# Optimization experiments

Measured on AMD Instinct MI355X. Metric: run time of the kernel, lower is better.

## Reference

```python
import jax, jax.numpy as jnp
import numpy as np

EPS = 1e-6

def _det3(m):
    return (m[..., 0, 0] * m[..., 1, 1] * m[..., 2, 2]
            + m[..., 0, 1] * m[..., 1, 2] * m[..., 2, 0]
            + m[..., 1, 0] * m[..., 2, 1] * m[..., 0, 2]
            - m[..., 2, 0] * m[..., 1, 1] * m[..., 0, 2]
            - m[..., 0, 0] * m[..., 2, 1] * m[..., 1, 2]
            - m[..., 1, 0] * m[..., 0, 1] * m[..., 2, 2])

def _inv3(m):
    a, b, c = m[..., 0, 0], m[..., 0, 1], m[..., 0, 2]
    d, e, f = m[..., 1, 0], m[..., 1, 1], m[..., 1, 2]
    g, h, i = m[..., 2, 0], m[..., 2, 1], m[..., 2, 2]
    adj = jnp.stack([
        jnp.stack([e * i - f * h, c * h - b * i, b * f - c * e], -1),
        jnp.stack([f * g - d * i, a * i - c * g, c * d - a * f], -1),
        jnp.stack([d * h - e * g, b * g - a * h, a * e - b * d], -1)], -2)
    return adj / _det3(m)[..., None, None]

def setup_inputs() -> dict:
    key = jax.random.key(0)
    ks = jax.random.split(key, 12)
    N, B, DH = 100000, 2048, 256
    idx = jnp.sort(jnp.concatenate([jnp.arange(B, dtype=jnp.int32),
                                    jax.random.randint(ks[0], (N - B,), 0, B, dtype=jnp.int32)]))
    return {
        "t": jax.random.uniform(ks[1], (B, 1), jnp.float32, 0.01, 0.99),
        "h": jax.random.normal(ks[2], (N, DH), jnp.float32),
        "pos": jax.random.normal(ks[3], (N, 3), jnp.float32),
        "eps_h": jax.random.normal(ks[4], (N, DH), jnp.float32),
        "eps_pos": jax.random.normal(ks[5], (N, 3), jnp.float32),
        "gparam_h": jax.random.normal(ks[6], (1, 1), jnp.float32),
        "gparam_pos": jax.random.normal(ks[7], (1, 1), jnp.float32),
        "W_mu": jax.random.normal(ks[8], (DH, DH), jnp.float32) / np.sqrt(DH),
        "W_r1": jax.random.normal(ks[9], (DH, 2 * DH), jnp.float32) / np.sqrt(DH),
        "W_r2": jax.random.normal(ks[10], (2 * DH, DH), jnp.float32) / np.sqrt(2 * DH),
        "index": idx,
        "num_graphs": B,
    }


def _forward(t, h, pos, eps_h, eps_pos, gparam_h, gparam_pos, W_mu, W_r1, W_r2, index, B):
    eye = jnp.eye(3, dtype=h.dtype)
    seg_sum = lambda x: jax.ops.segment_sum(x, index, num_segments=B)
    counts = seg_sum(jnp.ones((index.shape[0],), h.dtype))  # [B]

    def scatter_center(x):  # x - per-graph mean, gathered back
        mean = seg_sum(x) / counts[:, None]
        return x - mean[index]

    # volatility g(t): per-graph, gathered to nodes
    g_h = (0.1 + jax.nn.softplus(gparam_h) * t)[index]      # [N,1]
    g_pos = (0.1 + jax.nn.softplus(gparam_pos) * t)[index]  # [N,1]

    def f_net(t_, hh, pp):  # surrogate forward transformation f
        tn = t_[index]                                      # [N,1]
        mu_h = (hh @ W_mu) * (1.0 - tn)
        sigma_h = 0.1 + 0.9 * tn                            # [N,1]
        mu_pos = pp * (1.0 - tn)
        nrm = pp / (jnp.linalg.norm(pp, axis=-1, keepdims=True) + EPS)
        a = (0.2 + 0.8 * tn)[..., None]                     # [N,1,1]
        b = (0.1 * tn)[..., None]
        U = a * eye + b * (nrm[:, :, None] * nrm[:, None, :])  # [N,3,3]
        return mu_h, sigma_h, mu_pos, U

    def z_pos_fn(mu, U, eps):
        return mu + scatter_center(jnp.einsum('nij,nj->ni', U, eps))

    def score_pos_fn(eps, U, inv_U=None, C=None):
        if inv_U is None or C is None:
            inv_U = _inv3(U)
            inv_V = _inv3(seg_sum(inv_U))
            C = inv_V[index] @ (inv_U - eye)
        y = jnp.einsum('nji,nj->ni', inv_U, eps)
        ybar = seg_sum(y)
        c = jnp.einsum('nji,nj->ni', C, ybar[index])
        return scatter_center(c - y)  # zero_cog_score=True

    def solve_pos_fn(U, prel):
        inv_U = _inv3(U)
        inv_V = _inv3(seg_sum(inv_U))
        C = inv_V[index] @ (inv_U - eye)
        c = seg_sum(jnp.einsum('nij,nj->ni', C, prel))[index]
        eps = jnp.einsum('nij,nj->ni', inv_U, prel - c)
        return eps, inv_U, C

    bdrift = lambda dz, score, g: dz - 0.5 * g ** 2 * score

    # ---- target backward drift (time_derivative via jvp over t) ----
    (mu_h, sig_h, mu_p, U), (dmu_h, dsig_h, dmu_p, dU) = jax.jvp(
        lambda tt: f_net(tt, h, pos), (t,), (jnp.ones_like(t),))
    z_h = mu_h + sig_h * eps_h
    dz_h = dmu_h + dsig_h * eps_h
    z_p = z_pos_fn(mu_p, U, eps_pos)
    dz_p = z_pos_fn(dmu_p, dU, eps_pos)
    tgt_h = bdrift(dz_h, -eps_h / sig_h, g_h)
    tgt_p = bdrift(dz_p, score_pos_fn(eps_pos, U), g_pos)

    # ---- approximate backward drift ('x0' parameterization) ----
    h_r = jnp.tanh(z_h @ W_r1) @ W_r2   # reconstructor r
    pos_r = z_p * 0.9
    (mu_h2, sig_h2, mu_p2, U2), (dmu_h2, dsig_h2, dmu_p2, dU2) = jax.jvp(
        lambda tt: f_net(tt, h_r, pos_r), (t,), (jnp.ones_like(t),))
    eps_h2 = (z_h - mu_h2) / sig_h2
    eps_p2, inv_U2, C2 = solve_pos_fn(U2, z_p - mu_p2)
    dz_h2 = dmu_h2 + dsig_h2 * eps_h2
    dz_p2 = z_pos_fn(dmu_p2, dU2, eps_p2)
    apx_h = bdrift(dz_h2, -eps_h2 / sig_h2, g_h)
    apx_p = bdrift(dz_p2, score_pos_fn(eps_p2, U2, inv_U2, C2), g_pos)

    # ---- 'simple' loss: mse(approx/g, target/g) ----
    loss_h = jnp.mean(((apx_h - tgt_h) / g_h) ** 2)
    loss_p = jnp.mean(((apx_p - tgt_p) / g_pos) ** 2)
    return loss_h, loss_p


def reference(t, h, pos, eps_h, eps_pos, gparam_h, gparam_pos, W_mu, W_r1, W_r2, index, num_graphs):
    return _forward(t, h, pos, eps_h, eps_pos, gparam_h, gparam_pos, W_mu, W_r1, W_r2, index, num_graphs)
```

## Files before the change

### kernel.cpp

```cpp
#include <hip/hip_runtime.h>
#include <math.h>

#define NTHREADS 256
#define EPSC 1e-6f
#define NPL 3

typedef short bf16x8 __attribute__((ext_vector_type(8)));
typedef float f32x4  __attribute__((ext_vector_type(4)));

__device__ __forceinline__ ushort f2bf(float x) {
  union { float f; unsigned u; } v; v.f = x;
  unsigned r = v.u + 0x7FFFu + ((v.u >> 16) & 1u);
  return (ushort)(r >> 16);
}
__device__ __forceinline__ float bf2f(ushort x) {
  union { unsigned u; float f; } v; v.u = ((unsigned)x) << 16;
  return v.f;
}
__device__ __forceinline__ float tanh_fast(float x) {
  float xc = fminf(fmaxf(x, -15.f), 15.f);
  float e = __expf(2.f * xc);
  return (e - 1.f) / (e + 1.f);
}

__device__ __forceinline__ void inv3x3(const float m[9], float o[9]) {
  float a=m[0],b=m[1],c=m[2],d=m[3],e=m[4],f=m[5],g=m[6],h=m[7],i=m[8];
  float det = a*e*i + b*f*g + d*h*c - g*e*c - a*h*f - d*b*i;
  float r = 1.0f/det;
  o[0]=(e*i-f*h)*r; o[1]=(c*h-b*i)*r; o[2]=(b*f-c*e)*r;
  o[3]=(f*g-d*i)*r; o[4]=(a*i-c*g)*r; o[5]=(c*d-a*f)*r;
  o[6]=(d*h-e*g)*r; o[7]=(b*g-a*h)*r; o[8]=(a*e-b*d)*r;
}

__device__ __forceinline__ float wred(float v) {
#pragma unroll
  for (int o = 32; o > 0; o >>= 1) v += __shfl_xor(v, o, 64);
  return v;
}

__device__ __forceinline__ void block_reduce_atomic(double v, double* target) {
#pragma unroll
  for (int off = 32; off > 0; off >>= 1) v += __shfl_down(v, off, 64);
  __shared__ double sm[NTHREADS/64];
  int lane = threadIdx.x & 63, wv = threadIdx.x >> 6;
  if (lane == 0) sm[wv] = v;
  __syncthreads();
  if (threadIdx.x == 0) {
    double s = 0.0;
#pragma unroll
    for (int i = 0; i < NTHREADS/64; ++i) s += sm[i];
    atomicAdd(target, s);
  }
}

__global__ __launch_bounds__(64) void pos_fused(
    int N, const float* __restrict__ pos, const float* __restrict__ epsp,
    const int* __restrict__ index, const float* __restrict__ t,
    const float* __restrict__ gpp, double* __restrict__ lossp)
{
  const int b = blockIdx.x;
  const int lane = threadIdx.x;

  int lo = 0, hi = N;
  while (lo < hi) { int mid = (lo + hi) >> 1; if (index[mid] < b) lo = mid + 1; else hi = mid; }
  const int start = lo;
  hi = N;
  while (lo < hi) { int mid = (lo + hi) >> 1; if (index[mid] < b + 1) lo = mid + 1; else hi = mid; }
  const int end = lo;
  const int cnt = end - start;
  const float fn = (float)cnt, rc = 1.0f / fn;

  const float tn  = t[b];
  const float a1  = 0.2f + 0.8f*tn, b1 = 0.1f*tn;
  const float omt = 1.0f - tn;
  const float sp  = log1pf(expf(gpp[0]));
  const float gp  = 0.1f + sp*tn;
  const float hg  = 0.5f*gp*gp;
  const float rgp = 1.0f/gp;
  const float pscale = 1.0f - 0.9f*omt;

  float iU[NPL][9], yv[NPL][3], wv[NPL][3], dwv[NPL][3], pv[NPL][3];
  float Vs[9] = {0}, wb[3] = {0}, dwb[3] = {0}, yb[3] = {0};
#pragma unroll
  for (int k = 0; k < NPL; ++k) {
    const int n = start + k*64 + lane;
    if (n < end) {
      const float px = pos[3*(size_t)n+0], py = pos[3*(size_t)n+1], pz = pos[3*(size_t)n+2];
      const float ex = epsp[3*(size_t)n+0], ey = epsp[3*(size_t)n+1], ez = epsp[3*(size_t)n+2];
      pv[k][0]=px; pv[k][1]=py; pv[k][2]=pz;
      const float pn = sqrtf(px*px+py*py+pz*pz) + EPSC;
      const float nx = px/pn, ny = py/pn, nz = pz/pn;
      const float nd = nx*ex + ny*ey + nz*ez;
      wv[k][0]=a1*ex + b1*nd*nx; wv[k][1]=a1*ey + b1*nd*ny; wv[k][2]=a1*ez + b1*nd*nz;
      dwv[k][0]=0.8f*ex + 0.1f*nd*nx; dwv[k][1]=0.8f*ey + 0.1f*nd*ny; dwv[k][2]=0.8f*ez + 0.1f*nd*nz;
      const float U[9] = { a1 + b1*nx*nx, b1*nx*ny,      b1*nx*nz,
                           b1*ny*nx,      a1 + b1*ny*ny, b1*ny*nz,
                           b1*nz*nx,      b1*nz*ny,      a1 + b1*nz*nz };
      inv3x3(U, iU[k]);
      yv[k][0] = iU[k][0]*ex + iU[k][3]*ey + iU[k][6]*ez;
      yv[k][1] = iU[k][1]*ex + iU[k][4]*ey + iU[k][7]*ez;
      yv[k][2] = iU[k][2]*ex + iU[k][5]*ey + iU[k][8]*ez;
#pragma unroll
      for (int j = 0; j < 9; ++j) Vs[j] += iU[k][j];
#pragma unroll
      for (int j = 0; j < 3; ++j) { wb[j]+=wv[k][j]; dwb[j]+=dwv[k][j]; yb[j]+=yv[k][j]; }
    }
  }
#pragma unroll
  for (int j = 0; j < 9; ++j) Vs[j] = wred(Vs[j]);
#pragma unroll
  for (int j = 0; j < 3; ++j) { wb[j]=wred(wb[j]); dwb[j]=wred(dwb[j]); yb[j]=wred(yb[j]); }

  float iV[9]; inv3x3(Vs, iV);
  float wm[3], dwm[3], u1[3], s1m[3];
#pragma unroll
  for (int i = 0; i < 3; ++i) { wm[i] = wb[i]*rc; dwm[i] = dwb[i]*rc; }
#pragma unroll
  for (int i = 0; i < 3; ++i) u1[i] = iV[0*3+i]*yb[0] + iV[1*3+i]*yb[1] + iV[2*3+i]*yb[2];
#pragma unroll
  for (int i = 0; i < 3; ++i) {
    const float csy = Vs[0*3+i]*u1[0] + Vs[1*3+i]*u1[1] + Vs[2*3+i]*u1[2] - fn*u1[i];
    s1m[i] = (csy - yb[i]) * rc;
  }

  float tg[NPL][3], zp[NPL][3], iU2[NPL][9], qv[NPL][3];
  float Vs2[9] = {0}, qs[3] = {0}, ps[3] = {0};
#pragma unroll
  for (int k = 0; k < NPL; ++k) {
    const int n = start + k*64 + lane;
    if (n < end) {
#pragma unroll
      for (int i = 0; i < 3; ++i) {
        const float c1 = iU[k][0*3+i]*u1[0] + iU[k][1*3+i]*u1[1] + iU[k][2*3+i]*u1[2] - u1[i];
        const float score1 = c1 - yv[k][i] - s1m[i];
        tg[k][i] = -pv[k][i] + dwv[k][i] - dwm[i] - hg*score1;
        zp[k][i] = pv[k][i]*omt + wv[k][i] - wm[i];
      }
      const float rx = 0.9f*zp[k][0], ry = 0.9f*zp[k][1], rz = 0.9f*zp[k][2];
      const float rn = sqrtf(rx*rx+ry*ry+rz*rz) + EPSC;
      const float nx = rx/rn, ny = ry/rn, nz = rz/rn;
      const float U2[9] = { a1 + b1*nx*nx, b1*nx*ny,      b1*nx*nz,
                            b1*ny*nx,      a1 + b1*ny*ny, b1*ny*nz,
                            b1*nz*nx,      b1*nz*ny,      a1 + b1*nz*nz };
      inv3x3(U2, iU2[k]);
      float prel[3];
#pragma unroll
      for (int i = 0; i < 3; ++i) prel[i] = zp[k][i]*pscale;
#pragma unroll
      for (int i = 0; i < 3; ++i)
        qv[k][i] = iU2[k][i*3+0]*prel[0] + iU2[k][i*3+1]*prel[1] + iU2[k][i*3+2]*prel[2];
#pragma unroll
      for (int j = 0; j < 9; ++j) Vs2[j] += iU2[k][j];
#pragma unroll
      for (int j = 0; j < 3; ++j) { qs[j] += qv[k][j]; ps[j] += prel[j]; }
    }
  }
#pragma unroll
  for (int j = 0; j < 9; ++j) Vs2[j] = wred(Vs2[j]);
#pragma unroll
  for (int j = 0; j < 3; ++j) { qs[j] = wred(qs[j]); ps[j] = wred(ps[j]); }

  float iV2[9]; inv3x3(Vs2, iV2);
  float cb2[3];
#pragma unroll
  for (int i = 0; i < 3; ++i)
    cb2[i] = iV2[i*3+0]*(qs[0]-ps[0]) + iV2[i*3+1]*(qs[1]-ps[1]) + iV2[i*3+2]*(qs[2]-ps[2]);

  float y2v[NPL][3], dw2v[NPL][3];
  float yb2[3] = {0}, dwb2[3] = {0};
#pragma unroll
  for (int k = 0; k < NPL; ++k) {
    const int n = start + k*64 + lane;
    if (n < end) {
      float e[3];
#pragma unroll
      for (int i = 0; i < 3; ++i)
        e[i] = qv[k][i] - (iU2[k][i*3+0]*cb2[0] + iU2[k][i*3+1]*cb2[1] + iU2[k][i*3+2]*cb2[2]);
#pragma unroll
      for (int i = 0; i < 3; ++i)
        y2v[k][i] = iU2[k][0*3+i]*e[0] + iU2[k][1*3+i]*e[1] + iU2[k][2*3+i]*e[2];
      const float rx = 0.9f*zp[k][0], ry = 0.9f*zp[k][1], rz = 0.9f*zp[k][2];
      const float rn = sqrtf(rx*rx+ry*ry+rz*rz) + EPSC;
      const float nx = rx/rn, ny = ry/rn, nz = rz/rn;
      const float nd = nx*e[0] + ny*e[1] + nz*e[2];
      dw2v[k][0] = 0.8f*e[0] + 0.1f*nd*nx;
      dw2v[k][1] = 0.8f*e[1] + 0.1f*nd*ny;
      dw2v[k][2] = 0.8f*e[2] + 0.1f*nd*nz;
#pragma unroll
      for (int j = 0; j < 3; ++j) { yb2[j] += y2v[k][j]; dwb2[j] += dw2v[k][j]; }
    }
  }
#pragma unroll
  for (int j = 0; j < 3; ++j) { yb2[j] = wred(yb2[j]); dwb2[j] = wred(dwb2[j]); }

  float u2[3], s2m[3], dw2m[3];
#pragma unroll
  for (int i = 0; i < 3; ++i) u2[i] = iV2[0*3+i]*yb2[0] + iV2[1*3+i]*yb2[1] + iV2[2*3+i]*yb2[2];
#pragma unroll
  for (int i = 0; i < 3; ++i) {
    const float csy = Vs2[0*3+i]*u2[0] + Vs2[1*3+i]*u2[1] + Vs2[2*3+i]*u2[2] - fn*u2[i];
    s2m[i] = (csy - yb2[i]) * rc;
    dw2m[i] = dwb2[i] * rc;
  }

  float acc = 0.0f;
#pragma unroll
  for (int k = 0; k < NPL; ++k) {
    const int n = start + k*64 + lane;
    if (n < end) {
#pragma unroll
      for (int i = 0; i < 3; ++i) {
        const float c2 = iU2[k][0*3+i]*u2[0] + iU2[k][1*3+i]*u2[1] + iU2[k][2*3+i]*u2[2] - u2[i];
        const float score2 = c2 - y2v[k][i] - s2m[i];
        const float dz2 = -0.9f*zp[k][i] + dw2v[k][i] - dw2m[i];
        const float apx = dz2 - hg*score2;
        const float d = (apx - tg[k][i]) * rgp;
        acc += d*d;
      }
    }
  }
  acc = wred(acc);
  if (lane == 0) atomicAdd(lossp, (double)acc);
}

__global__ __launch_bounds__(NTHREADS) void cvt_bf16(
    const float4* __restrict__ in, ushort4* __restrict__ out, int n4)
{
  for (int i = blockIdx.x*blockDim.x + threadIdx.x; i < n4; i += gridDim.x*blockDim.x) {
    float4 v = in[i];
    out[i] = make_ushort4(f2bf(v.x), f2bf(v.y), f2bf(v.z), f2bf(v.w));
  }
}

__global__ __launch_bounds__(NTHREADS) void transpose_cvt(
    const float* __restrict__ in, ushort* __restrict__ out, int K, int Nn)
{
  __shared__ float ts[32][33];
  const int tx = threadIdx.x & 31, ty = threadIdx.x >> 5;
  const int nb = blockIdx.x*32, kb = blockIdx.y*32;
#pragma unroll
  for (int r = 0; r < 4; ++r)
    ts[ty + r*8][tx] = in[(size_t)(kb + ty + r*8)*Nn + nb + tx];
  __syncthreads();
#pragma unroll
  for (int r = 0; r < 4; ++r)
    out[(size_t)(nb + ty + r*8)*K + kb + tx] = f2bf(ts[tx][ty + r*8]);
}

template<int EPI>
__global__ __launch_bounds__(256) void gemm_mfma(
    const ushort* __restrict__ A, const ushort* __restrict__ Bt,
    int K, int Nn, int Mvalid,
    ushort* __restrict__ OutB, ushort* __restrict__ OutB2,
    const float* __restrict__ eps, const int* __restrict__ index,
    const float* __restrict__ t, const float* __restrict__ gph,
    const ushort* __restrict__ HmIn, double* __restrict__ lossAcc)
{
  __shared__ __align__(16) ushort As[128*32];
  __shared__ __align__(16) ushort Bs[128*32];
  const int tid = threadIdx.x;
  const int row0 = blockIdx.y*128, col0 = blockIdx.x*128;
  const int wave = tid >> 6, lane = tid & 63;
  const int wm = (wave & 1)*64, wn = (wave >> 1)*64;
  const int lm = lane & 15, lq = lane >> 4;

  f32x4 acc[4][4];
#pragma unroll
  for (int i = 0; i < 4; ++i)
#pragma unroll
    for (int j = 0; j < 4; ++j) { acc[i][j][0]=0.f; acc[i][j][1]=0.f; acc[i][j][2]=0.f; acc[i][j][3]=0.f; }

  const int c0 = tid, c1 = tid + 256;
  const int r0a = c0 >> 2, k0a = (c0 & 3) << 3;
  const int r1a = c1 >> 2, k1a = (c1 & 3) << 3;

  for (int k0 = 0; k0 < K; k0 += 32) {
    __syncthreads();
    __builtin_amdgcn_global_load_lds(
        (const __attribute__((address_space(1))) void*)(A + (size_t)(row0 + r0a)*K + k0 + k0a),
        (__attribute__((address_space(3))) void*)(As + c0*8), 16, 0, 0);
    __builtin_amdgcn_global_load_lds(
        (const __attribute__((address_space(1))) void*)(A + (size_t)(row0 + r1a)*K + k0 + k1a),
        (__attribute__((address_space(3))) void*)(As + c1*8), 16, 0, 0);
    __builtin_amdgcn_global_load_lds(
        (const __attribute__((address_space(1))) void*)(Bt + (size_t)(col0 + r0a)*K + k0 + k0a),
        (__attribute__((address_space(3))) void*)(Bs + c0*8), 16, 0, 0);
    __builtin_amdgcn_global_load_lds(
        (const __attribute__((address_space(1))) void*)(Bt + (size_t)(col0 + r1a)*K + k0 + k1a),
        (__attribute__((address_space(3))) void*)(Bs + c1*8), 16, 0, 0);
    __syncthreads();

    bf16x8 af[4], bfr[4];
#pragma unroll
    for (int i = 0; i < 4; ++i)
      af[i] = *(const bf16x8*)&As[(wm + i*16 + lm)*32 + lq*8];
#pragma unroll
    for (int j = 0; j < 4; ++j)
      bfr[j] = *(const bf16x8*)&Bs[(wn + j*16 + lm)*32 + lq*8];
#pragma unroll
    for (int i = 0; i < 4; ++i)
#pragma unroll
      for (int j = 0; j < 4; ++j)
        acc[i][j] = __builtin_amdgcn_mfma_f32_16x16x32_bf16(af[i], bfr[j], acc[i][j], 0, 0, 0);
  }

  if constexpr (EPI == 3) {
    const float sp = log1pf(expf(gph[0]));
    float local = 0.f;
#pragma unroll
    for (int i = 0; i < 4; ++i) {
#pragma unroll
      for (int reg = 0; reg < 4; ++reg) {
        const int r = row0 + wm + i*16 + lq*4 + reg;
        if (r < Mvalid) {
          const float tn = t[index[r]];
          const float gh  = 0.1f + sp*tn;
          const float sig = 0.1f + 0.9f*tn;
          const float fac = 1.0f + (0.9f + 0.5f*gh*gh/sig)*(1.0f - tn)/sig;
          const float sc  = fac/gh;
#pragma unroll
          for (int j = 0; j < 4; ++j) {
            const int cc = col0 + wn + j*16 + lm;
            const float d = (bf2f(HmIn[(size_t)r*Nn + cc]) - acc[i][j][reg]) * sc;
            local += d*d;
          }
        }
      }
    }
    block_reduce_atomic((double)local, lossAcc);
  } else if constexpr (EPI == 1) {
#pragma unroll
    for (int i = 0; i < 4; ++i) {
#pragma unroll
      for (int reg = 0; reg < 4; ++reg) {
        const int r  = row0 + wm + i*16 + lq*4 + reg;
        const int rcl = (r < Mvalid) ? r : (Mvalid - 1);
        const float tn = t[index[rcl]];
        const float s0 = 1.0f - tn, s1 = 0.1f + 0.9f*tn;
#pragma unroll
        for (int j = 0; j < 4; ++j) {
          const int cc = col0 + wn + j*16 + lm;
          const float v = acc[i][j][reg];
          OutB2[(size_t)r*Nn + cc] = f2bf(v);
          OutB [(size_t)r*Nn + cc] = f2bf(v*s0 + s1*eps[(size_t)rcl*Nn + cc]);
        }
      }
    }
  } else if constexpr (EPI == 4) {
#pragma unroll
    for (int i = 0; i < 4; ++i) {
#pragma unroll
      for (int reg = 0; reg < 4; ++reg) {
        const int r = row0 + wm + i*16 + lq*4 + reg;
#pragma unroll
        for (int j = 0; j < 4; ++j) {
          const int cc = col0 + wn + j*16 + lm;
          OutB[(size_t)cc*Mvalid + r] = f2bf(acc[i][j][reg]);
        }
      }
    }
  } else {
#pragma unroll
    for (int i = 0; i < 4; ++i) {
#pragma unroll
      for (int reg = 0; reg < 4; ++reg) {
        const int r = row0 + wm + i*16 + lq*4 + reg;
#pragma unroll
        for (int j = 0; j < 4; ++j) {
          const int cc = col0 + wn + j*16 + lm;
          OutB[(size_t)r*Nn + cc] = f2bf(tanh_fast(acc[i][j][reg]));
        }
      }
    }
  }
}

__global__ void finalize_kernel(const double* lossh, const double* lossp,
                                float* out, int N, int DH)
{
  if (threadIdx.x == 0) {
    out[0] = (float)(lossh[0] / ((double)N * (double)DH));
    out[1] = (float)(lossp[0] / ((double)N * 3.0));
  }
}

extern "C" void kernel_launch(void* const* d_in, const int* in_sizes, int n_in,
                              void* d_out, int out_size, void* d_ws, size_t ws_size,
                              hipStream_t stream) {
  const float* t      = (const float*)d_in[0];
  const float* h      = (const float*)d_in[1];
  const float* pos    = (const float*)d_in[2];
  const float* eps_h  = (const float*)d_in[3];
  const float* eps_p  = (const float*)d_in[4];
  const float* gph    = (const float*)d_in[5];
  const float* gpp    = (const float*)d_in[6];
  const float* W_mu   = (const float*)d_in[7];
  const float* W_r1   = (const float*)d_in[8];
  const float* W_r2   = (const float*)d_in[9];
  const int*   index  = (const int*)d_in[10];
  const int B = in_sizes[0];
  const int N = in_sizes[10];
  const int DH = 256, DH2 = 512;
  const int NPAD = 100352;

  char* ws = (char*)d_ws;
  size_t off = 0;
  auto alloc = [&](size_t nbytes) { size_t o = off; off += (nbytes + 255) & ~(size_t)255; return o; };

  size_t o_loss = alloc(16);
  size_t o_hb   = alloc((size_t)NPAD*DH*2);
  size_t o_wmut = alloc((size_t)DH*DH*2);
  size_t o_wr1t = alloc((size_t)DH2*DH*2);
  size_t o_wr2b = alloc((size_t)DH2*DH*2);
  size_t o_wct  = alloc((size_t)DH*DH2*2);
  size_t o_HmB  = alloc((size_t)NPAD*DH*2);
  size_t o_zh   = alloc((size_t)NPAD*DH*2);
  size_t o_T1   = alloc((size_t)NPAD*DH2*2);

  hipMemsetAsync(ws + o_loss, 0, 16, stream);

  double* lossh = (double*)(ws + o_loss);
  double* lossp = lossh + 1;
  ushort* hb   = (ushort*)(ws + o_hb);
  ushort* wmut = (ushort*)(ws + o_wmut);
  ushort* wr1t = (ushort*)(ws + o_wr1t);
  ushort* wr2b = (ushort*)(ws + o_wr2b);
  ushort* wct  = (ushort*)(ws + o_wct);
  ushort* HmB  = (ushort*)(ws + o_HmB);
  ushort* zh   = (ushort*)(ws + o_zh);
  ushort* T1   = (ushort*)(ws + o_T1);

  pos_fused<<<B, 64, 0, stream>>>(N, pos, eps_p, index, t, gpp, lossp);

  cvt_bf16<<<2048, NTHREADS, 0, stream>>>((const float4*)h, (ushort4*)hb, N*DH/4);
  cvt_bf16<<<128, NTHREADS, 0, stream>>>((const float4*)W_r2, (ushort4*)wr2b, DH2*DH/4);
  transpose_cvt<<<dim3(DH/32,  DH/32), NTHREADS, 0, stream>>>(W_mu, wmut, DH, DH);
  transpose_cvt<<<dim3(DH2/32, DH/32), NTHREADS, 0, stream>>>(W_r1, wr1t, DH, DH2);

  gemm_mfma<4><<<dim3(DH/128, DH2/128), 256, 0, stream>>>(
      wr2b, wmut, DH, DH, DH2,
      wct, nullptr, nullptr, nullptr, nullptr, nullptr, nullptr, nullptr);

  const int mg = (N + 127) / 128;
  gemm_mfma<1><<<dim3(DH/128, mg), 256, 0, stream>>>(
      hb, wmut, DH, DH, N,
      zh, HmB, eps_h, index, t, nullptr, nullptr, nullptr);
  gemm_mfma<2><<<dim3(DH2/128, mg), 256, 0, stream>>>(
      zh, wr1t, DH, DH2, N,
      T1, nullptr, nullptr, nullptr, nullptr, nullptr, nullptr, nullptr);
  gemm_mfma<3><<<dim3(DH/128, mg), 256, 0, stream>>>(
      T1, wct, DH2, DH, N,
      nullptr, nullptr, nullptr, index, t, gph, HmB, lossh);

  finalize_kernel<<<1, 64, 0, stream>>>(lossh, lossp, (float*)d_out, N, DH);
}
```

Before: 505.0 us.

## Fuse h-branch GEMM chain into one kernel keeping intermediates in LDS

Replaces the three separate row-tiled GEMM launches (h@W_mu with noise mixing, z_h@W_r1 with tanh, T1@Wcomb with loss) by one kernel that processes 32 rows per block and keeps z_h and T1 tiles in shared memory. The fp32-to-bf16 conversion of h is folded into the first GEMM's load, and the Hm buffer is kept in registers for the loss. This removes large global-memory writes and reads of intermediates, but each block restages all weight tiles, which raises L2 traffic and adds frequent block-wide barriers. It also assumes N is a multiple of 32.

```diff
diff --git a/kernel.cpp b/kernel.cpp
--- a/kernel.cpp
+++ b/kernel.cpp
@@ -4,6 +4,10 @@
 #define NTHREADS 256
 #define EPSC 1e-6f
 #define NPL 3
+
+#define MB 32
+#define PZ 264
+#define PB 40
 
 typedef short bf16x8 __attribute__((ext_vector_type(8)));
 typedef float f32x4  __attribute__((ext_vector_type(4)));
@@ -12,10 +16,6 @@
   union { float f; unsigned u; } v; v.f = x;
   unsigned r = v.u + 0x7FFFu + ((v.u >> 16) & 1u);
   return (ushort)(r >> 16);
-}
-__device__ __forceinline__ float bf2f(ushort x) {
-  union { unsigned u; float f; } v; v.u = ((unsigned)x) << 16;
-  return v.f;
 }
 __device__ __forceinline__ float tanh_fast(float x) {
   float xc = fminf(fmaxf(x, -15.f), 15.f);
@@ -247,14 +247,9 @@
     out[(size_t)(nb + ty + r*8)*K + kb + tx] = f2bf(ts[tx][ty + r*8]);
 }
 
-template<int EPI>
-__global__ __launch_bounds__(256) void gemm_mfma(
+__global__ __launch_bounds__(256) void gemm_wcomb(
     const ushort* __restrict__ A, const ushort* __restrict__ Bt,
-    int K, int Nn, int Mvalid,
-    ushort* __restrict__ OutB, ushort* __restrict__ OutB2,
-    const float* __restrict__ eps, const int* __restrict__ index,
-    const float* __restrict__ t, const float* __restrict__ gph,
-    const ushort* __restrict__ HmIn, double* __restrict__ lossAcc)
+    int K, int Nn, int Mvalid, ushort* __restrict__ OutB)
 {
   __shared__ __align__(16) ushort As[128*32];
   __shared__ __align__(16) ushort Bs[128*32];
@@ -303,75 +298,143 @@
       for (int j = 0; j < 4; ++j)
         acc[i][j] = __builtin_amdgcn_mfma_f32_16x16x32_bf16(af[i], bfr[j], acc[i][j], 0, 0, 0);
   }
-
-  if constexpr (EPI == 3) {
-    const float sp = log1pf(expf(gph[0]));
-    float local = 0.f;
-#pragma unroll
-    for (int i = 0; i < 4; ++i) {
-#pragma unroll
-      for (int reg = 0; reg < 4; ++reg) {
-        const int r = row0 + wm + i*16 + lq*4 + reg;
-        if (r < Mvalid) {
-          const float tn = t[index[r]];
-          const float gh  = 0.1f + sp*tn;
-          const float sig = 0.1f + 0.9f*tn;
-          const float fac = 1.0f + (0.9f + 0.5f*gh*gh/sig)*(1.0f - tn)/sig;
-          const float sc  = fac/gh;
-#pragma unroll
-          for (int j = 0; j < 4; ++j) {
-            const int cc = col0 + wn + j*16 + lm;
-            const float d = (bf2f(HmIn[(size_t)r*Nn + cc]) - acc[i][j][reg]) * sc;
-            local += d*d;
-          }
-        }
+#pragma unroll
+  for (int i = 0; i < 4; ++i)
+#pragma unroll
+    for (int reg = 0; reg < 4; ++reg) {
+      const int r = row0 + wm + i*16 + lq*4 + reg;
+#pragma unroll
+      for (int j = 0; j < 4; ++j) {
+        const int cc = col0 + wn + j*16 + lm;
+        OutB[(size_t)cc*Mvalid + r] = f2bf(acc[i][j][reg]);
       }
     }
-    block_reduce_atomic((double)local, lossAcc);
-  } else if constexpr (EPI == 1) {
-#pragma unroll
-    for (int i = 0; i < 4; ++i) {
-#pragma unroll
-      for (int reg = 0; reg < 4; ++reg) {
-        const int r  = row0 + wm + i*16 + lq*4 + reg;
-        const int rcl = (r < Mvalid) ? r : (Mvalid - 1);
-        const float tn = t[index[rcl]];
-        const float s0 = 1.0f - tn, s1 = 0.1f + 0.9f*tn;
-#pragma unroll
-        for (int j = 0; j < 4; ++j) {
-          const int cc = col0 + wn + j*16 + lm;
-          const float v = acc[i][j][reg];
-          OutB2[(size_t)r*Nn + cc] = f2bf(v);
-          OutB [(size_t)r*Nn + cc] = f2bf(v*s0 + s1*eps[(size_t)rcl*Nn + cc]);
-        }
-      }
-    }
-  } else if constexpr (EPI == 4) {
-#pragma unroll
-    for (int i = 0; i < 4; ++i) {
-#pragma unroll
-      for (int reg = 0; reg < 4; ++reg) {
-        const int r = row0 + wm + i*16 + lq*4 + reg;
-#pragma unroll
-        for (int j = 0; j < 4; ++j) {
-          const int cc = col0 + wn + j*16 + lm;
-          OutB[(size_t)cc*Mvalid + r] = f2bf(acc[i][j][reg]);
-        }
-      }
-    }
-  } else {
-#pragma unroll
-    for (int i = 0; i < 4; ++i) {
-#pragma unroll
-      for (int reg = 0; reg < 4; ++reg) {
-        const int r = row0 + wm + i*16 + lq*4 + reg;
-#pragma unroll
-        for (int j = 0; j < 4; ++j) {
-          const int cc = col0 + wn + j*16 + lm;
-          OutB[(size_t)r*Nn + cc] = f2bf(tanh_fast(acc[i][j][reg]));
-        }
-      }
-    }
+}
+
+__global__ __launch_bounds__(512, 4) void mega_h(
+    const float* __restrict__ h, const float* __restrict__ eps,
+    const ushort* __restrict__ wmut, const ushort* __restrict__ wr1t,
+    const ushort* __restrict__ wct,
+    const int* __restrict__ index, const float* __restrict__ t,
+    const float* __restrict__ gph, double* __restrict__ lossh)
+{
+  __shared__ __align__(16) ushort zhL[MB*PZ];
+  __shared__ __align__(16) ushort T1L[MB*PZ];
+  __shared__ __align__(16) ushort Bst[1280*8];
+  __shared__ double smr[8];
+
+  const int tid  = threadIdx.x;
+  const int wave = tid >> 6, lane = tid & 63;
+  const int lm = lane & 15, lq = lane >> 4;
+  const int rowbase = (wave & 1) * 16;
+  const int colbase = (wave >> 1) * 64;
+  const int row0g = blockIdx.x * MB;
+
+  float tn[4];
+#pragma unroll
+  for (int reg = 0; reg < 4; ++reg)
+    tn[reg] = t[index[row0g + rowbase + lq*4 + reg]];
+
+  auto stageB = [&](const ushort* src, int ldb, int kw) {
+    for (int c = tid; c < 1280; c += 512) {
+      int outer = c / 5;
+      int sub = c - outer*5; sub = (sub == 4) ? 0 : sub;
+      __builtin_amdgcn_global_load_lds(
+          (const __attribute__((address_space(1))) void*)(src + (size_t)outer*ldb + kw + sub*8),
+          (__attribute__((address_space(3))) void*)(Bst + c*8), 16, 0, 0);
+    }
+  };
+  auto mfmaStep = [&](const ushort* Abase, int apitch, int aoff, f32x4 acc[4]) {
+    bf16x8 af = *(const bf16x8*)&Abase[(rowbase + lm)*apitch + aoff + lq*8];
+#pragma unroll
+    for (int j = 0; j < 4; ++j) {
+      bf16x8 bfv = *(const bf16x8*)&Bst[(colbase + j*16 + lm)*PB + lq*8];
+      acc[j] = __builtin_amdgcn_mfma_f32_16x16x32_bf16(af, bfv, acc[j], 0, 0, 0);
+    }
+  };
+
+  f32x4 hm[4];
+#pragma unroll
+  for (int j = 0; j < 4; ++j) { hm[j][0]=0.f; hm[j][1]=0.f; hm[j][2]=0.f; hm[j][3]=0.f; }
+
+  {
+    const int arow = tid >> 4, ac2 = (tid & 15) * 2;
+    for (int kw = 0; kw < 256; kw += 32) {
+      __syncthreads();
+      float2 hv = *(const float2*)&h[(size_t)(row0g + arow)*256 + kw + ac2];
+      ushort2 hp; hp.x = f2bf(hv.x); hp.y = f2bf(hv.y);
+      *(ushort2*)&T1L[arow*PB + ac2] = hp;
+      stageB(wmut, 256, kw);
+      __syncthreads();
+      mfmaStep(T1L, PB, 0, hm);
+    }
+  }
+
+#pragma unroll
+  for (int reg = 0; reg < 4; ++reg) {
+    const int rl = rowbase + lq*4 + reg;
+    const float s0 = 1.0f - tn[reg], s1 = 0.1f + 0.9f*tn[reg];
+#pragma unroll
+    for (int j = 0; j < 4; ++j) {
+      const int cl = colbase + j*16 + lm;
+      const float e = eps[(size_t)(row0g + rl)*256 + cl];
+      zhL[rl*PZ + cl] = f2bf(hm[j][reg]*s0 + s1*e);
+    }
+  }
+
+  f32x4 hm2[4];
+#pragma unroll
+  for (int j = 0; j < 4; ++j) { hm2[j][0]=0.f; hm2[j][1]=0.f; hm2[j][2]=0.f; hm2[j][3]=0.f; }
+
+  for (int half = 0; half < 2; ++half) {
+    f32x4 t1a[4];
+#pragma unroll
+    for (int j = 0; j < 4; ++j) { t1a[j][0]=0.f; t1a[j][1]=0.f; t1a[j][2]=0.f; t1a[j][3]=0.f; }
+    for (int kw = 0; kw < 256; kw += 32) {
+      __syncthreads();
+      stageB(wr1t + (size_t)half*256*256, 256, kw);
+      __syncthreads();
+      mfmaStep(zhL, PZ, kw, t1a);
+    }
+#pragma unroll
+    for (int reg = 0; reg < 4; ++reg) {
+      const int rl = rowbase + lq*4 + reg;
+#pragma unroll
+      for (int j = 0; j < 4; ++j)
+        T1L[rl*PZ + colbase + j*16 + lm] = f2bf(tanh_fast(t1a[j][reg]));
+    }
+    for (int kw = 0; kw < 256; kw += 32) {
+      __syncthreads();
+      stageB(wct + half*256, 512, kw);
+      __syncthreads();
+      mfmaStep(T1L, PZ, kw, hm2);
+    }
+  }
+
+  const float sp = log1pf(expf(gph[0]));
+  float local = 0.0f;
+#pragma unroll
+  for (int reg = 0; reg < 4; ++reg) {
+    const float gh  = 0.1f + sp*tn[reg];
+    const float sig = 0.1f + 0.9f*tn[reg];
+    const float fac = 1.0f + (0.9f + 0.5f*gh*gh/sig)*(1.0f - tn[reg])/sig;
+    const float sc  = fac/gh;
+#pragma unroll
+    for (int j = 0; j < 4; ++j) {
+      const float d = (hm[j][reg] - hm2[j][reg]) * sc;
+      local += d*d;
+    }
+  }
+  double v = (double)local;
+#pragma unroll
+  for (int off = 32; off > 0; off >>= 1) v += __shfl_down(v, off, 64);
+  if (lane == 0) smr[wave] = v;
+  __syncthreads();
+  if (tid == 0) {
+    double s = 0.0;
+#pragma unroll
+    for (int i = 0; i < 8; ++i) s += smr[i];
+    atomicAdd(lossh, s);
   }
 }
 
@@ -401,56 +464,34 @@
   const int B = in_sizes[0];
   const int N = in_sizes[10];
   const int DH = 256, DH2 = 512;
-  const int NPAD = 100352;
 
   char* ws = (char*)d_ws;
   size_t off = 0;
   auto alloc = [&](size_t nbytes) { size_t o = off; off += (nbytes + 255) & ~(size_t)255; return o; };
 
   size_t o_loss = alloc(16);
-  size_t o_hb   = alloc((size_t)NPAD*DH*2);
   size_t o_wmut = alloc((size_t)DH*DH*2);
   size_t o_wr1t = alloc((size_t)DH2*DH*2);
   size_t o_wr2b = alloc((size_t)DH2*DH*2);
   size_t o_wct  = alloc((size_t)DH*DH2*2);
-  size_t o_HmB  = alloc((size_t)NPAD*DH*2);
-  size_t o_zh   = alloc((size_t)NPAD*DH*2);
-  size_t o_T1   = alloc((size_t)NPAD*DH2*2);
 
   hipMemsetAsync(ws + o_loss, 0, 16, stream);
 
   double* lossh = (double*)(ws + o_loss);
   double* lossp = lossh + 1;
-  ushort* hb   = (ushort*)(ws + o_hb);
   ushort* wmut = (ushort*)(ws + o_wmut);
   ushort* wr1t = (ushort*)(ws + o_wr1t);
   ushort* wr2b = (ushort*)(ws + o_wr2b);
   ushort* wct  = (ushort*)(ws + o_wct);
-  ushort* HmB  = (ushort*)(ws + o_HmB);
-  ushort* zh   = (ushort*)(ws + o_zh);
-  ushort* T1   = (ushort*)(ws + o_T1);
 
   pos_fused<<<B, 64, 0, stream>>>(N, pos, eps_p, index, t, gpp, lossp);
 
-  cvt_bf16<<<2048, NTHREADS, 0, stream>>>((const float4*)h, (ushort4*)hb, N*DH/4);
   cvt_bf16<<<128, NTHREADS, 0, stream>>>((const float4*)W_r2, (ushort4*)wr2b, DH2*DH/4);
   transpose_cvt<<<dim3(DH/32,  DH/32), NTHREADS, 0, stream>>>(W_mu, wmut, DH, DH);
   transpose_cvt<<<dim3(DH2/32, DH/32), NTHREADS, 0, stream>>>(W_r1, wr1t, DH, DH2);
-
-  gemm_mfma<4><<<dim3(DH/128, DH2/128), 256, 0, stream>>>(
-      wr2b, wmut, DH, DH, DH2,
-      wct, nullptr, nullptr, nullptr, nullptr, nullptr, nullptr, nullptr);
-
-  const int mg = (N + 127) / 128;
-  gemm_mfma<1><<<dim3(DH/128, mg), 256, 0, stream>>>(
-      hb, wmut, DH, DH, N,
-      zh, HmB, eps_h, index, t, nullptr, nullptr, nullptr);
-  gemm_mfma<2><<<dim3(DH2/128, mg), 256, 0, stream>>>(
-      zh, wr1t, DH, DH2, N,
-      T1, nullptr, nullptr, nullptr, nullptr, nullptr, nullptr, nullptr);
-  gemm_mfma<3><<<dim3(DH/128, mg), 256, 0, stream>>>(
-      T1, wct, DH2, DH, N,
-      nullptr, nullptr, nullptr, index, t, gph, HmB, lossh);
+  gemm_wcomb<<<dim3(DH/128, DH2/128), 256, 0, stream>>>(wr2b, wmut, DH, DH, DH2, wct);
+
+  mega_h<<<N/MB, 512, 0, stream>>>(h, eps_h, wmut, wr1t, wct, index, t, gph, lossh);
 
   finalize_kernel<<<1, 64, 0, stream>>>(lossh, lossp, (float*)d_out, N, DH);
 }
```

New measurement: 506.5 us. No clear change (+0.3%).
